# Kernel tuning notes

Hardware: AMD Instinct MI355X
Metric: run time of the kernel (lower is better)

The kernel has to match this reference:

```python
import jax, jax.numpy as jnp
import numpy as np

ITERATIONS = 100  # resonator iterations (default in __init__)


def _quantize(x):
    # MAP/bipolar quantize: sign with ties -> +1
    return jnp.where(x >= 0, 1.0, -1.0).astype(x.dtype)


def _resonator_step(inp, estimates, codebooks):
    # inp: (b, d); estimates: (b, f, d); codebooks: (f, v, d)
    f = estimates.shape[-2]
    # rolled copies, stacked: (b, f, f-1, d); product = multibind of all other factors
    rolled = jnp.stack([jnp.roll(estimates, i, axis=-3 + 1) for i in range(1, f)], axis=-2)
    inv_others = jnp.prod(rolled, axis=-2)              # (b, f, d)
    new_estimates = inp[:, None, :] * inv_others        # bind, (b, f, d)
    similarity = jnp.einsum('bfd,fvd->bfv', new_estimates, codebooks)  # (b, f, v)
    # multiset with similarity weights, then quantize
    output = _quantize(jnp.einsum('bfv,fvd->bfd', similarity, codebooks))
    max_sim = jnp.max(similarity, axis=-1)              # (b, f)
    return output, max_sim


def setup_inputs() -> dict:
    key = jax.random.key(0)
    b, f, v, d = 1024, 4, 64, 2048
    k1, k2 = jax.random.split(key)
    # bipolar codebooks (f, v, d)
    codebooks = _quantize(jax.random.normal(k1, (f, v, d), dtype=jnp.float32))
    # construct a solvable input: bind of one random codevector per factor
    idx = jax.random.randint(k2, (b, f), 0, v)          # (b, f)
    chosen = codebooks[jnp.arange(f)[None, :], idx]     # (b, f, d)
    inp = jnp.prod(chosen, axis=1)                      # (b, d)
    # init estimates: quantized multiset (bundle) of each codebook, tiled over batch
    init = _quantize(jnp.sum(codebooks, axis=1))        # (f, d)
    init_estimates = jnp.broadcast_to(init[None], (b, f, d)).astype(jnp.float32)
    return {"input": inp, "init_estimates": init_estimates, "codebooks": codebooks}


def reference(input, init_estimates, codebooks):
    # Concurrent resonator network, fixed iteration count (data-dependent
    # early-convergence check omitted for jit compatibility).
    def body(est, _):
        out, max_sim = _resonator_step(input, est, codebooks)
        return out, max_sim

    estimates, max_sims = jax.lax.scan(body, init_estimates, None, length=ITERATIONS)
    # cleanup: argmax of |similarity| against codebooks (argmax_abs=True)
    sim = jnp.einsum('bfd,fvd->bfv', estimates, codebooks)
    outcome = jnp.argmax(jnp.abs(sim), axis=-1).astype(jnp.int32)  # (b, f)
    convergence = jnp.int32(ITERATIONS - 1)
    return estimates, outcome, max_sims[-1], convergence
```

## Files before the change

### kernel.cpp

```cpp
#include <hip/hip_runtime.h>
#include <stdint.h>


#define NB 1024
#define NF 4
#define ND 2048
#define NW 32
#define ITERS 100
#define NRB 4

#define OFF_OUT  (NB*NF*ND)
#define OFF_MS   (OFF_OUT + NB*NF)
#define OFF_CONV (OFF_MS + NB*NF)

typedef unsigned long long u64;

__global__ void pack_cb_kernel(const float* __restrict__ cb,
                               u64* __restrict__ cbB, u64* __restrict__ cbT) {
    const int lane = threadIdx.x & 63;
    const int gw   = (blockIdx.x * (blockDim.x >> 6)) + (threadIdx.x >> 6);
    const int nw   = (gridDim.x * blockDim.x) >> 6;
    for (int idx = gw; idx < NF * 64 * NW; idx += nw) {
        const int j = idx >> 11, v = (idx >> 5) & 63, w = idx & 31;
        const float x = cb[(((j << 6) | v) << 11) + (w << 6) + lane];
        const u64 m = __ballot(x < 0.0f);
        if (lane == 0)
            cbB[(((((j << 4) | (w >> 1)) << 6) | v) << 1) | (w & 1)] = m;
    }
    for (int idx = gw; idx < NF * ND; idx += nw) {
        const int j = idx >> 11, d = idx & 2047;
        const float x = cb[(((j << 6) | lane) << 11) + d];
        const u64 m = __ballot(x < 0.0f);
        const int w = d >> 6, la = d & 63;
        if (lane == 0)
            cbT[(((((j << 4) | (w >> 1)) << 6) | la) << 1) | (w & 1)] = m;
    }
}

#define PCW(CW, W)                                                           \
    {                                                                        \
        const u64 cw_ = (CW);                                                \
        int t = base + cmul * (int)__popcll(cw_);                            \
        t += (int)__popcll(c0 & cw_) << 2;                                   \
        t += (int)__popcll(c1 & cw_) << 3;                                   \
        t += (int)__popcll(c2 & cw_) << 4;                                   \
        t += (int)__popcll(c3 & cw_) << 5;                                   \
        t += (int)__popcll(c4 & cw_) << 6;                                   \
        t += (int)__popcll(c5 & cw_) << 7;                                   \
        t += (int)__popcll(c6 & cw_) << 8;                                   \
        t += (int)__popcll(c7 & cw_) << 9;                                   \
        t += oe0 * (int)((cw_ >> ov0) & 1);                                  \
        t += oe1 * (int)((cw_ >> ov1) & 1);                                  \
        if (nov > 2) {                              \
            u64 m2 = om;                                                     \
            while (m2) {                                                     \
                const int vv = __builtin_ctzll(m2); m2 &= m2 - 1;            \
                t += 4 * __builtin_amdgcn_readlane(ex, vv)                   \
                       * (int)((cw_ >> vv) & 1);                             \
            }                                                                \
        }                                                                    \
        const u64 nww = __ballot(t < 0);                                     \
        if (lane == 0) s_hist[r][nxt][j][W] = nww;                           \
    }

__global__ __launch_bounds__(1024, 4) void resonator_kernel(
    const float* __restrict__ inp, const float* __restrict__ est_init,
    const u64* __restrict__ cbB, const u64* __restrict__ cbT,
    float* __restrict__ out) {
    __shared__ u64 l_cbB[NF * 16 * 64 * 2];
    __shared__ u64 l_cbT[NF * 16 * 64 * 2];
    __shared__ u64 s_hist[NRB][3][NF][NW];
    __shared__ u64 s_inp[NRB][NW];
    __shared__ u64 s_ne[NRB][NF][NW];
    __shared__ int s_conv[NRB][NF];
    __shared__ int s_fs[NRB];

    const int b    = blockIdx.x;
    const int tid  = threadIdx.x;
    const int wid  = tid >> 6;
    const int lane = tid & 63;
    const int j    = wid & 3;
    const int r    = wid >> 2;
    const int row  = (b << 2) + r;

    for (int idx = tid; idx < NF * 16 * 64 * 2; idx += 1024) {
        l_cbB[idx] = cbB[idx];
        l_cbT[idx] = cbT[idx];
    }
    #pragma unroll
    for (int k = 0; k < 8; ++k) {
        const int w = (j << 3) + k;
        const u64 m = __ballot(inp[(row << 11) + (w << 6) + lane] < 0.0f);
        if (lane == 0) s_inp[r][w] = m;
    }
    #pragma unroll 4
    for (int w = 0; w < NW; ++w) {
        const u64 m = __ballot(
            est_init[(((row << 2) | j) << 11) + (w << 6) + lane] < 0.0f);
        if (lane == 0) s_hist[r][0][j][w] = m;
    }
    __syncthreads();

    const ulonglong2* tB = (const ulonglong2*)l_cbB + (j << 10) + lane;
    const ulonglong2* tT = (const ulonglong2*)l_cbT + (j << 10) + lane;

    int ml = 0, mp = 0, fs = 0;
    int cur = 0, nxt = 1, prv = 2;

    for (int it = 0; it < ITERS; ++it) {
        if (lane < NW) {
            const u64 X = s_inp[r][lane]
                ^ s_hist[r][cur][0][lane] ^ s_hist[r][cur][1][lane]
                ^ s_hist[r][cur][2][lane] ^ s_hist[r][cur][3][lane];
            s_ne[r][j][lane] = X ^ s_hist[r][cur][j][lane];
        }

        int pc = 0;
        #pragma unroll
        for (int w2 = 0; w2 < 16; ++w2) {
            const ulonglong2 g  = tB[w2 << 6];
            const ulonglong2 nn = *(const ulonglong2*)&s_ne[r][j][w2 << 1];
            pc += (int)__popcll(nn.x ^ g.x) + (int)__popcll(nn.y ^ g.y);
        }
        int mn = pc, sp = pc;
        #pragma unroll
        for (int off = 32; off > 0; off >>= 1) {
            const int a1 = __shfl_xor(mn, off);
            const int a2 = __shfl_xor(sp, off);
            mn = mn < a1 ? mn : a1;
            sp += a2;
        }
        mp = ml; ml = ND - 2 * mn;

        const int mean = sp >> 6;
        const int dev  = pc - mean;
        const int devc = dev < -128 ? -128 : (dev > 127 ? 127 : dev);
        const int ex   = dev - devc;
        const int u    = devc + 128;
        const u64 c0 = __ballot(u & 1),  c1 = __ballot(u & 2);
        const u64 c2 = __ballot(u & 4),  c3 = __ballot(u & 8);
        const u64 c4 = __ballot(u & 16), c5 = __ballot(u & 32);
        const u64 c6 = __ballot(u & 64), c7 = __ballot(u & 128);
        u64 om = __ballot(ex != 0);
        const int nov = (int)__popcll(om);
        int ov0 = 0, ov1 = 0, oe0 = 0, oe1 = 0;
        if (nov > 0) {
            ov0 = __builtin_ctzll(om); om &= om - 1;
            oe0 = 4 * __builtin_amdgcn_readlane(ex, ov0);
            if (nov > 1) {
                ov1 = __builtin_ctzll(om); om &= om - 1;
                oe1 = 4 * __builtin_amdgcn_readlane(ex, ov1);
            }
        }
        const int base = 131072 - 2 * sp;
        const int cmul = 4 * mean - 4608;

        #pragma unroll
        for (int w2 = 0; w2 < 16; ++w2) {
            const ulonglong2 g = tT[w2 << 6];
            PCW(g.x, (w2 << 1))
            PCW(g.y, (w2 << 1) + 1)
        }

        int d1 = 0, d2 = 0;
        if (lane < NW) {
            const u64 a = s_hist[r][nxt][j][lane];
            d1 = (a != s_hist[r][cur][j][lane]);
            d2 = (a != s_hist[r][prv][j][lane]);
        }
        const u64 b1 = __ballot(d1), b2 = __ballot(d2);
        if (lane == 0) s_conv[r][j] = (b1 == 0 ? 1 : 0) | (b2 == 0 ? 2 : 0);
        __syncthreads();

        int flr = 0;
        bool allok = true;
        #pragma unroll
        for (int r2 = 0; r2 < NRB; ++r2) {
            const int f = s_conv[r2][0] & s_conv[r2][1]
                        & s_conv[r2][2] & s_conv[r2][3];
            if (r2 == r) flr = f;
            allok = allok && ((f & 1) || (it >= 1 && (f & 2)));
        }
        fs = nxt;
        if (allok) {
            if (!(flr & 1) && ((ITERS - it) & 1) == 0) { fs = cur; ml = mp; }
            break;
        }
        const int t3 = prv; prv = cur; cur = nxt; nxt = t3;
    }

    if (j == 0 && lane == 0) s_fs[r] = fs;

    int pcO = 0;
    #pragma unroll
    for (int w2 = 0; w2 < 16; ++w2) {
        const ulonglong2 g  = tB[w2 << 6];
        const ulonglong2 hh = *(const ulonglong2*)&s_hist[r][fs][j][w2 << 1];
        pcO += (int)__popcll(hh.x ^ g.x) + (int)__popcll(hh.y ^ g.y);
    }
    const int simF = ND - (pcO << 1);
    const int aF   = simF < 0 ? -simF : simF;
    int key = (aF << 6) | (63 - lane);
    #pragma unroll
    for (int off = 32; off > 0; off >>= 1) {
        const int t1 = __shfl_xor(key, off);
        key = key > t1 ? key : t1;
    }
    if (lane == 0) {
        out[OFF_OUT + (row << 2) + j] = (float)(63 - (key & 63));
        out[OFF_MS  + (row << 2) + j] = (float)ml;
    }
    __syncthreads();

    #pragma unroll
    for (int rr = 0; rr < NRB; ++rr) {
        const int f2 = s_fs[rr];
        #pragma unroll
        for (int k = 0; k < 8; ++k) {
            const int idx = tid + (k << 10);
            const int jj = idx >> 11, d = idx & 2047;
            const u64 wrd = s_hist[rr][f2][jj][d >> 6];
            out[(((b << 2) + rr) << 13) + idx] =
                ((wrd >> (d & 63)) & 1) ? -1.0f : 1.0f;
        }
    }
    if (b == 0 && tid == 0) out[OFF_CONV] = 99.0f;
}

extern "C" void kernel_launch(void* const* d_in, const int* in_sizes, int n_in,
                              void* d_out, int out_size, void* d_ws, size_t ws_size,
                              hipStream_t stream) {
    const float* inp  = (const float*)d_in[0];
    const float* est0 = (const float*)d_in[1];
    const float* cb   = (const float*)d_in[2];
    float* out = (float*)d_out;
    u64* cbB = (u64*)d_ws;
    u64* cbT = cbB + NF * 16 * 64 * 2;

    pack_cb_kernel<<<64, 256, 0, stream>>>(cb, cbB, cbT);
    resonator_kernel<<<NB / NRB, 1024, 0, stream>>>(inp, est0, cbB, cbT, out);
}
```

Measured before the change: 1.673 ms.

## Move max-similarity reduction out of the iteration loop and batch codebook loads

Drops the per-iteration min-reduction that tracked the maximum similarity. After the loop it recomputes max_sim once from the saved state of the previous iteration. The codebook loads from LDS are split into two batches of eight vector registers so they can be issued before the popcount work. Launch bounds are relaxed from 4 to 2 waves per SIMD, which gives the compiler more registers but may reduce occupancy.

```diff
diff --git a/kernel.cpp b/kernel.cpp
--- a/kernel.cpp
+++ b/kernel.cpp
@@ -63,7 +63,7 @@
         if (lane == 0) s_hist[r][nxt][j][W] = nww;                           \
     }
 
-__global__ __launch_bounds__(1024, 4) void resonator_kernel(
+__global__ __launch_bounds__(1024, 2) void resonator_kernel(
     const float* __restrict__ inp, const float* __restrict__ est_init,
     const u64* __restrict__ cbB, const u64* __restrict__ cbT,
     float* __restrict__ out) {
@@ -104,7 +104,7 @@
     const ulonglong2* tB = (const ulonglong2*)l_cbB + (j << 10) + lane;
     const ulonglong2* tT = (const ulonglong2*)l_cbT + (j << 10) + lane;
 
-    int ml = 0, mp = 0, fs = 0;
+    int s100 = -1, s99 = -1;
     int cur = 0, nxt = 1, prv = 2;
 
     for (int it = 0; it < ITERS; ++it) {
@@ -117,20 +117,23 @@
 
         int pc = 0;
         #pragma unroll
-        for (int w2 = 0; w2 < 16; ++w2) {
-            const ulonglong2 g  = tB[w2 << 6];
-            const ulonglong2 nn = *(const ulonglong2*)&s_ne[r][j][w2 << 1];
-            pc += (int)__popcll(nn.x ^ g.x) + (int)__popcll(nn.y ^ g.y);
-        }
-        int mn = pc, sp = pc;
-        #pragma unroll
-        for (int off = 32; off > 0; off >>= 1) {
-            const int a1 = __shfl_xor(mn, off);
-            const int a2 = __shfl_xor(sp, off);
-            mn = mn < a1 ? mn : a1;
-            sp += a2;
-        }
-        mp = ml; ml = ND - 2 * mn;
+        for (int hh = 0; hh < 2; ++hh) {
+            ulonglong2 gB[8];
+            #pragma unroll
+            for (int k = 0; k < 8; ++k)
+                gB[k] = tB[((hh << 3) | k) << 6];
+            #pragma unroll
+            for (int k = 0; k < 8; ++k) {
+                const int w2 = (hh << 3) | k;
+                const ulonglong2 nn =
+                    *(const ulonglong2*)&s_ne[r][j][w2 << 1];
+                pc += (int)__popcll(nn.x ^ gB[k].x)
+                    + (int)__popcll(nn.y ^ gB[k].y);
+            }
+        }
+        int sp = pc;
+        #pragma unroll
+        for (int off = 32; off > 0; off >>= 1) sp += __shfl_xor(sp, off);
 
         const int mean = sp >> 6;
         const int dev  = pc - mean;
@@ -156,10 +159,17 @@
         const int cmul = 4 * mean - 4608;
 
         #pragma unroll
-        for (int w2 = 0; w2 < 16; ++w2) {
-            const ulonglong2 g = tT[w2 << 6];
-            PCW(g.x, (w2 << 1))
-            PCW(g.y, (w2 << 1) + 1)
+        for (int hh = 0; hh < 2; ++hh) {
+            ulonglong2 gT[8];
+            #pragma unroll
+            for (int k = 0; k < 8; ++k)
+                gT[k] = tT[((hh << 3) | k) << 6];
+            #pragma unroll
+            for (int k = 0; k < 8; ++k) {
+                const int w2 = (hh << 3) | k;
+                PCW(gT[k].x, (w2 << 1))
+                PCW(gT[k].y, (w2 << 1) + 1)
+            }
         }
 
         int d1 = 0, d2 = 0;
@@ -181,21 +191,25 @@
             if (r2 == r) flr = f;
             allok = allok && ((f & 1) || (it >= 1 && (f & 2)));
         }
-        fs = nxt;
         if (allok) {
-            if (!(flr & 1) && ((ITERS - it) & 1) == 0) { fs = cur; ml = mp; }
+            if (flr & 1) { s100 = nxt; s99 = nxt; }
+            else {
+                s100 = (((ITERS - it) & 1) == 0) ? cur : nxt;
+                s99  = (s100 == nxt) ? cur : nxt;
+            }
             break;
         }
         const int t3 = prv; prv = cur; cur = nxt; nxt = t3;
     }
-
-    if (j == 0 && lane == 0) s_fs[r] = fs;
+    if (s100 < 0) { s100 = cur; s99 = prv; }
+
+    if (j == 0 && lane == 0) s_fs[r] = s100;
 
     int pcO = 0;
     #pragma unroll
     for (int w2 = 0; w2 < 16; ++w2) {
         const ulonglong2 g  = tB[w2 << 6];
-        const ulonglong2 hh = *(const ulonglong2*)&s_hist[r][fs][j][w2 << 1];
+        const ulonglong2 hh = *(const ulonglong2*)&s_hist[r][s100][j][w2 << 1];
         pcO += (int)__popcll(hh.x ^ g.x) + (int)__popcll(hh.y ^ g.y);
     }
     const int simF = ND - (pcO << 1);
@@ -206,9 +220,31 @@
         const int t1 = __shfl_xor(key, off);
         key = key > t1 ? key : t1;
     }
+
+    int pc9 = 0;
+    #pragma unroll
+    for (int w2 = 0; w2 < 16; ++w2) {
+        const ulonglong2 g = tB[w2 << 6];
+        const int w = w2 << 1;
+        const u64 X0 = s_inp[r][w]
+            ^ s_hist[r][s99][0][w] ^ s_hist[r][s99][1][w]
+            ^ s_hist[r][s99][2][w] ^ s_hist[r][s99][3][w];
+        const u64 n0 = X0 ^ s_hist[r][s99][j][w];
+        const u64 X1 = s_inp[r][w + 1]
+            ^ s_hist[r][s99][0][w + 1] ^ s_hist[r][s99][1][w + 1]
+            ^ s_hist[r][s99][2][w + 1] ^ s_hist[r][s99][3][w + 1];
+        const u64 n1 = X1 ^ s_hist[r][s99][j][w + 1];
+        pc9 += (int)__popcll(n0 ^ g.x) + (int)__popcll(n1 ^ g.y);
+    }
+    int mn9 = pc9;
+    #pragma unroll
+    for (int off = 32; off > 0; off >>= 1) {
+        const int a1 = __shfl_xor(mn9, off);
+        mn9 = mn9 < a1 ? mn9 : a1;
+    }
     if (lane == 0) {
         out[OFF_OUT + (row << 2) + j] = (float)(63 - (key & 63));
-        out[OFF_MS  + (row << 2) + j] = (float)ml;
+        out[OFF_MS  + (row << 2) + j] = (float)(ND - 2 * mn9);
     }
     __syncthreads();
 
```

New measurement: 1.632 ms. -2.5%, faster.
